# Kernel tuning notes

Measured on AMD Instinct MI355X. Metric: run time of the kernel, lower is better.

## Reference

```python
import jax, jax.numpy as jnp
import numpy as np

B, NS, D, H = 1024, 32, 1024, 4096
LN_EPS = 1e-5


def _layer_norm(x, g, b):
    mu = jnp.mean(x, axis=-1, keepdims=True)
    var = jnp.mean(jnp.square(x - mu), axis=-1, keepdims=True)
    return (x - mu) * jax.lax.rsqrt(var + LN_EPS) * g + b


def setup_inputs() -> dict:
    key = jax.random.key(0)
    ks = jax.random.split(key, 12)
    sc = 0.02
    inp = {
        "x": jax.random.normal(ks[0], (B, D), jnp.float32),
        "S": jax.random.normal(ks[1], (B, NS, D), jnp.float32),
        # route_mlp: Linear(2D, D) -> GELU -> Linear(D, NS)
        "w_r1": jax.random.normal(ks[2], (2 * D, D), jnp.float32) * sc,
        "b_r1": jnp.zeros((D,), jnp.float32),
        "w_r2": jax.random.normal(ks[3], (D, NS), jnp.float32) * sc,
        "b_r2": jnp.zeros((NS,), jnp.float32),
        # GRUCell(D, D): gates ordered [r, z, n] as in torch
        "w_ih": jax.random.normal(ks[4], (D, 3 * D), jnp.float32) * sc,
        "w_hh": jax.random.normal(ks[5], (D, 3 * D), jnp.float32) * sc,
        "b_ih": jnp.zeros((3 * D,), jnp.float32),
        "b_hh": jnp.zeros((3 * D,), jnp.float32),
        # slot_proj: Linear(D, D)
        "w_proj": jax.random.normal(ks[6], (D, D), jnp.float32) * sc,
        "b_proj": jnp.zeros((D,), jnp.float32),
        # ln1 / ffn / ln2
        "ln1_g": jnp.ones((D,), jnp.float32),
        "ln1_b": jnp.zeros((D,), jnp.float32),
        "w_f1": jax.random.normal(ks[7], (D, H), jnp.float32) * sc,
        "b_f1": jnp.zeros((H,), jnp.float32),
        "w_f2": jax.random.normal(ks[8], (H, D), jnp.float32) * sc,
        "b_f2": jnp.zeros((D,), jnp.float32),
        "ln2_g": jnp.ones((D,), jnp.float32),
        "ln2_b": jnp.zeros((D,), jnp.float32),
    }
    return inp


def reference(x, S, w_r1, b_r1, w_r2, b_r2, w_ih, w_hh, b_ih, b_hh,
              w_proj, b_proj, ln1_g, ln1_b, w_f1, b_f1, w_f2, b_f2,
              ln2_g, ln2_b):
    tau = 1.0
    # --- context-aware routing ---
    slot_mean = jnp.mean(S, axis=1)                     # [B, D]
    ctx = jnp.concatenate([x, slot_mean], axis=-1)      # [B, 2D]
    h_r = jax.nn.gelu(ctx @ w_r1 + b_r1, approximate=False)
    r_logits = h_r @ w_r2 + b_r2                        # [B, NS]
    alpha = jax.nn.softmax(r_logits / tau, axis=-1)     # [B, NS]

    # --- GRU slot update: input U = alpha * x broadcast over slots ---
    U = alpha[:, :, None] * x[:, None, :]               # [B, NS, D]
    gi = U @ w_ih + b_ih                                # [B, NS, 3D]
    gh = S @ w_hh + b_hh                                # [B, NS, 3D]
    gi_r, gi_z, gi_n = jnp.split(gi, 3, axis=-1)
    gh_r, gh_z, gh_n = jnp.split(gh, 3, axis=-1)
    r = jax.nn.sigmoid(gi_r + gh_r)
    z = jax.nn.sigmoid(gi_z + gh_z)
    n = jnp.tanh(gi_n + r * gh_n)
    S_new = (1.0 - z) * n + z * S                       # [B, NS, D]

    # --- weighted readout (slot_dropout = 0.0) ---
    slot_context = jnp.sum(alpha[:, :, None] * S_new, axis=1)  # [B, D]
    slot_update = slot_context @ w_proj + b_proj
    x_mid = x + slot_update

    # --- FFN + residual + LayerNorms ---
    h = _layer_norm(x_mid, ln1_g, ln1_b)
    ff = jax.nn.gelu(h @ w_f1 + b_f1, approximate=False) @ w_f2 + b_f2
    x_out = _layer_norm(x_mid + ff, ln2_g, ln2_b)
    return (x_out, S_new, alpha)
```

## Files before the change

kernel.cpp:

```cpp
#include <hip/hip_runtime.h>
#include <hip/hip_bf16.h>

#define BB 1024
#define NSLOT 32
#define DD 1024
#define HH 4096

typedef __bf16 bfx8 __attribute__((ext_vector_type(8)));
typedef float f32x4 __attribute__((ext_vector_type(4)));

__device__ __forceinline__ unsigned short f2bfu(float f) {
  union { float f; unsigned u; } v; v.f = f;
  unsigned r = v.u + 0x7fffu + ((v.u >> 16) & 1u);
  return (unsigned short)(r >> 16);
}
__device__ __forceinline__ float bfu2f(unsigned short u) {
  union { unsigned u; float f; } v; v.u = ((unsigned)u) << 16; return v.f;
}
__device__ __forceinline__ float gelu_f(float x) {
  return 0.5f * x * (1.0f + erff(x * 0.70710678118654752f));
}
__device__ __forceinline__ float sigm(float x) { return 1.0f / (1.0f + expf(-x)); }

__device__ __forceinline__ void async16(const unsigned short* g, unsigned short* l) {
  __builtin_amdgcn_global_load_lds(
      (const __attribute__((address_space(1))) unsigned int*)g,
      (__attribute__((address_space(3))) unsigned int*)l, 16, 0, 0);
}


__global__ __launch_bounds__(256) void cvt_x_ctx(const float* __restrict__ x,
                                                 unsigned short* __restrict__ ctx) {
  int i = blockIdx.x * 256 + threadIdx.x;
  int b = i >> 8;
  int c4 = (i & 255) * 4;
  float4 v = ((const float4*)(x + (size_t)b * DD))[i & 255];
  ushort4 o; o.x = f2bfu(v.x); o.y = f2bfu(v.y); o.z = f2bfu(v.z); o.w = f2bfu(v.w);
  *(ushort4*)&ctx[(size_t)b * (2 * DD) + c4] = o;
}

__global__ __launch_bounds__(256) void cvt4(const float* __restrict__ in,
                                            unsigned short* __restrict__ out, int n4) {
  int i = blockIdx.x * 256 + threadIdx.x;
  if (i >= n4) return;
  float4 v = ((const float4*)in)[i];
  ushort4 o; o.x = f2bfu(v.x); o.y = f2bfu(v.y); o.z = f2bfu(v.z); o.w = f2bfu(v.w);
  ((ushort4*)out)[i] = o;
}

__global__ __launch_bounds__(256) void slot_mean_k(const unsigned short* __restrict__ Sb,
                                                   unsigned short* __restrict__ ctx) {
  int i = blockIdx.x * 256 + threadIdx.x;
  int b = i >> 10, d = i & 1023;
  const unsigned short* p = Sb + (size_t)b * NSLOT * DD + d;
  float s = 0.f;
  #pragma unroll
  for (int sl = 0; sl < NSLOT; sl++) s += bfu2f(p[sl * DD]);
  ctx[(size_t)b * (2 * DD) + DD + d] = f2bfu(s * (1.0f / NSLOT));
}

__global__ __launch_bounds__(256) void transp(const float* __restrict__ in,
                                              unsigned short* __restrict__ out,
                                              int R, int C) {
  __shared__ float t[32][33];
  int tx = threadIdx.x & 31, ty = threadIdx.x >> 5;
  int c0 = blockIdx.x * 32, r0 = blockIdx.y * 32;
  #pragma unroll
  for (int i = 0; i < 4; i++) {
    int r = r0 + ty * 4 + i;
    t[ty * 4 + i][tx] = in[(size_t)r * C + c0 + tx];
  }
  __syncthreads();
  #pragma unroll
  for (int i = 0; i < 4; i++) {
    int c = c0 + ty * 4 + i;
    out[(size_t)c * R + r0 + tx] = f2bfu(t[tx][ty * 4 + i]);
  }
}

template <int EPI>
__global__ __launch_bounds__(256) void gemm_nt(
    const unsigned short* __restrict__ A, int lda,
    const unsigned short* __restrict__ Bt, int ldb, int K,
    const float* __restrict__ bias,
    const float* __restrict__ add, int ldadd,
    float* __restrict__ outF, unsigned short* __restrict__ outB, int ldout) {
  __shared__ __align__(16) unsigned short lA[128 * 40];
  __shared__ __align__(16) unsigned short lB[64 * 40];
  const int tid = threadIdx.x;
  const int wave = tid >> 6, lane = tid & 63;
  const int q = lane >> 4, l15 = lane & 15;
  const int row0 = blockIdx.y * 128;
  const int col0 = blockIdx.x * 64;
  const int ar = tid >> 2;
  const int ac = (tid & 3) * 8;

  f32x4 acc[2][4];
  #pragma unroll
  for (int m = 0; m < 2; m++)
    #pragma unroll
    for (int n = 0; n < 4; n++) acc[m][n] = (f32x4){0.f, 0.f, 0.f, 0.f};

  for (int k0 = 0; k0 < K; k0 += 32) {
    *(uint4*)&lA[ar * 40 + ac] = *(const uint4*)&A[(size_t)(row0 + ar) * lda + k0 + ac];
    *(uint4*)&lA[(ar + 64) * 40 + ac] = *(const uint4*)&A[(size_t)(row0 + ar + 64) * lda + k0 + ac];
    *(uint4*)&lB[ar * 40 + ac] = *(const uint4*)&Bt[(size_t)(col0 + ar) * ldb + k0 + ac];
    __syncthreads();
    bfx8 af[2], bf[4];
    #pragma unroll
    for (int m = 0; m < 2; m++)
      af[m] = *(const bfx8*)&lA[(wave * 32 + m * 16 + l15) * 40 + q * 8];
    #pragma unroll
    for (int n = 0; n < 4; n++)
      bf[n] = *(const bfx8*)&lB[(n * 16 + l15) * 40 + q * 8];
    #pragma unroll
    for (int m = 0; m < 2; m++)
      #pragma unroll
      for (int n = 0; n < 4; n++)
        acc[m][n] = __builtin_amdgcn_mfma_f32_16x16x32_bf16(af[m], bf[n], acc[m][n], 0, 0, 0);
    __syncthreads();
  }

  #pragma unroll
  for (int m = 0; m < 2; m++) {
    #pragma unroll
    for (int n = 0; n < 4; n++) {
      int gr0 = row0 + wave * 32 + m * 16 + q * 4;
      int gc = col0 + n * 16 + l15;
      #pragma unroll
      for (int i = 0; i < 4; i++) {
        int gr = gr0 + i;
        float v = acc[m][n][i];
        if (EPI == 0) {
          outF[(size_t)gr * ldout + gc] = v;
        } else if (EPI == 1) {
          float t = gelu_f(v + bias[gc]);
          outB[(size_t)gr * ldout + gc] = f2bfu(t);
        } else {
          outF[(size_t)gr * ldout + gc] = v + bias[gc] + add[(size_t)gr * ldadd + gc];
        }
      }
    }
  }
}

__global__ __launch_bounds__(256) void gru_gemm(
    const unsigned short* __restrict__ Sb, const unsigned short* __restrict__ Whht,
    const float* __restrict__ alpha, const float* __restrict__ xw,
    const float* __restrict__ b_ih, const float* __restrict__ b_hh,
    const float* __restrict__ Sf, float* __restrict__ Snew,
    unsigned short* __restrict__ sc_b) {
  __shared__ __align__(16) unsigned short lA[2][128 * 32];
  __shared__ __align__(16) unsigned short lB[2][192 * 32];
  const int tid = threadIdx.x;
  const int wave = tid >> 6, lane = tid & 63;
  const int wr = wave >> 1, wc = wave & 1;
  const int q = lane >> 4, l15 = lane & 15;
  const int row0 = blockIdx.y * 128;
  const int col0 = blockIdx.x * 64;
  const int halfA = 128 * 32, halfB = 192 * 32;

  const int lr = lane >> 2, scn = lane & 3;
  const unsigned short* aSrc[2];
  unsigned short* aDst[2];
  #pragma unroll
  for (int j = 0; j < 2; j++) {
    int R0 = (2 * wave + j) * 16;
    int r = R0 + lr;
    int c = scn ^ ((r >> 1) & 3);
    aSrc[j] = Sb + (size_t)(row0 + r) * DD + c * 8;
    aDst[j] = &lA[0][R0 * 32];
  }
  const unsigned short* bSrc[3];
  unsigned short* bDst[3];
  #pragma unroll
  for (int j = 0; j < 3; j++) {
    int R0 = (3 * wave + j) * 16;
    int r = R0 + lr;
    int g = r >> 6, cr = r & 63;
    int c = scn ^ ((r >> 1) & 3);
    bSrc[j] = Whht + ((size_t)g * DD + col0 + cr) * DD + c * 8;
    bDst[j] = &lB[0][R0 * 32];
  }

  int offA[4];
  #pragma unroll
  for (int m = 0; m < 4; m++) {
    int r = wr * 64 + m * 16 + l15;
    offA[m] = r * 32 + (q ^ ((r >> 1) & 3)) * 8;
  }
  int offB[3][2];
  #pragma unroll
  for (int g = 0; g < 3; g++)
    #pragma unroll
    for (int n = 0; n < 2; n++) {
      int r = g * 64 + wc * 32 + n * 16 + l15;
      offB[g][n] = r * 32 + (q ^ ((r >> 1) & 3)) * 8;
    }

  f32x4 acc[3][4][2];
  #pragma unroll
  for (int g = 0; g < 3; g++)
    #pragma unroll
    for (int m = 0; m < 4; m++)
      #pragma unroll
      for (int n = 0; n < 2; n++) acc[g][m][n] = (f32x4){0.f, 0.f, 0.f, 0.f};

  for (int it = 0; it < 16; it++) {
    #pragma unroll
    for (int j = 0; j < 2; j++) {
      async16(aSrc[j], aDst[j]);
      async16(aSrc[j] + 32, aDst[j] + halfA);
      aSrc[j] += 64;
    }
    #pragma unroll
    for (int j = 0; j < 3; j++) {
      async16(bSrc[j], bDst[j]);
      async16(bSrc[j] + 32, bDst[j] + halfB);
      bSrc[j] += 64;
    }
    __syncthreads();
    #pragma unroll
    for (int h = 0; h < 2; h++) {
      bfx8 af[4];
      #pragma unroll
      for (int m = 0; m < 4; m++) af[m] = *(const bfx8*)&lA[h][offA[m]];
      #pragma unroll
      for (int g = 0; g < 3; g++) {
        bfx8 bf0 = *(const bfx8*)&lB[h][offB[g][0]];
        bfx8 bf1 = *(const bfx8*)&lB[h][offB[g][1]];
        #pragma unroll
        for (int m = 0; m < 4; m++) {
          acc[g][m][0] = __builtin_amdgcn_mfma_f32_16x16x32_bf16(af[m], bf0, acc[g][m][0], 0, 0, 0);
          acc[g][m][1] = __builtin_amdgcn_mfma_f32_16x16x32_bf16(af[m], bf1, acc[g][m][1], 0, 0, 0);
        }
      }
    }
    __syncthreads();
  }

  float scp[2][2] = {{0.f, 0.f}, {0.f, 0.f}};
  #pragma unroll
  for (int m = 0; m < 4; m++) {
    #pragma unroll
    for (int i = 0; i < 4; i++) {
      int gr = row0 + wr * 64 + m * 16 + q * 4 + i;
      float a = alpha[gr];
      const float* xwr = xw + (size_t)(gr >> 5) * (3 * DD);
      const float* sfr = Sf + (size_t)gr * DD;
      float* orow = Snew + (size_t)gr * DD;
      #pragma unroll
      for (int n = 0; n < 2; n++) {
        int gc = col0 + wc * 32 + n * 16 + l15;
        float ghr = acc[0][m][n][i] + b_hh[gc];
        float ghz = acc[1][m][n][i] + b_hh[gc + DD];
        float ghn = acc[2][m][n][i] + b_hh[gc + 2 * DD];
        float r = sigm(a * xwr[gc] + b_ih[gc] + ghr);
        float z = sigm(a * xwr[gc + DD] + b_ih[gc + DD] + ghz);
        float nn = tanhf(a * xwr[gc + 2 * DD] + b_ih[gc + 2 * DD] + r * ghn);
        float sv = (1.0f - z) * nn + z * sfr[gc];
        orow[gc] = sv;
        scp[m >> 1][n] += a * sv;
      }
    }
  }
  #pragma unroll
  for (int bh = 0; bh < 2; bh++)
    #pragma unroll
    for (int n = 0; n < 2; n++) {
      float v = scp[bh][n];
      v += __shfl_xor(v, 16);
      v += __shfl_xor(v, 32);
      if (q == 0) {
        int batch = (row0 >> 5) + wr * 2 + bh;
        int gc = col0 + wc * 32 + n * 16 + l15;
        sc_b[(size_t)batch * DD + gc] = f2bfu(v);
      }
    }
}

__global__ __launch_bounds__(256) void route_softmax(
    const unsigned short* __restrict__ h_r, const float* __restrict__ w_r2,
    const float* __restrict__ b_r2, float* __restrict__ alpha_out) {
  int b = blockIdx.x;
  int n = threadIdx.x & 31, c = threadIdx.x >> 5;
  __shared__ float part[8][32];
  __shared__ float logits[32];
  const unsigned short* hr = h_r + (size_t)b * DD;
  float s = 0.f;
  for (int i = 0; i < 128; i++) {
    int k = c * 128 + i;
    s += bfu2f(hr[k]) * w_r2[k * NSLOT + n];
  }
  part[c][n] = s;
  __syncthreads();
  if (threadIdx.x < 32) {
    float t = b_r2[n];
    #pragma unroll
    for (int cc = 0; cc < 8; cc++) t += part[cc][n];
    logits[n] = t;
  }
  __syncthreads();
  if (threadIdx.x < 32) {
    float mx = -1e30f;
    #pragma unroll
    for (int j = 0; j < 32; j++) mx = fmaxf(mx, logits[j]);
    float den = 0.f;
    #pragma unroll
    for (int j = 0; j < 32; j++) den += expf(logits[j] - mx);
    alpha_out[(size_t)b * NSLOT + n] = expf(logits[n] - mx) / den;
  }
}

template <int OUT_BF>
__global__ __launch_bounds__(256) void ln_k(const float* __restrict__ in,
                                            const float* __restrict__ gw,
                                            const float* __restrict__ bw,
                                            float* __restrict__ outF,
                                            unsigned short* __restrict__ outB) {
  int b = blockIdx.x;
  int tid = threadIdx.x;
  float4 v = ((const float4*)(in + (size_t)b * DD))[tid];
  float s = v.x + v.y + v.z + v.w;
  float s2 = v.x * v.x + v.y * v.y + v.z * v.z + v.w * v.w;
  #pragma unroll
  for (int o = 32; o > 0; o >>= 1) { s += __shfl_down(s, o); s2 += __shfl_down(s2, o); }
  __shared__ float as1[4], as2[4];
  int wave = tid >> 6, lane = tid & 63;
  if (lane == 0) { as1[wave] = s; as2[wave] = s2; }
  __syncthreads();
  float t1 = as1[0] + as1[1] + as1[2] + as1[3];
  float t2 = as2[0] + as2[1] + as2[2] + as2[3];
  float mu = t1 * (1.0f / DD);
  float var = t2 * (1.0f / DD) - mu * mu;
  float rstd = rsqrtf(var + 1e-5f);
  int d = tid * 4;
  float o0 = (v.x - mu) * rstd * gw[d] + bw[d];
  float o1 = (v.y - mu) * rstd * gw[d + 1] + bw[d + 1];
  float o2 = (v.z - mu) * rstd * gw[d + 2] + bw[d + 2];
  float o3 = (v.w - mu) * rstd * gw[d + 3] + bw[d + 3];
  if (OUT_BF) {
    ushort4 o; o.x = f2bfu(o0); o.y = f2bfu(o1); o.z = f2bfu(o2); o.w = f2bfu(o3);
    *(ushort4*)&outB[(size_t)b * DD + d] = o;
  } else {
    float4 o; o.x = o0; o.y = o1; o.z = o2; o.w = o3;
    *(float4*)&outF[(size_t)b * DD + d] = o;
  }
}

extern "C" void kernel_launch(void* const* d_in, const int* in_sizes, int n_in,
                              void* d_out, int out_size, void* d_ws, size_t ws_size,
                              hipStream_t stream) {
  const float* x      = (const float*)d_in[0];
  const float* S      = (const float*)d_in[1];
  const float* w_r1   = (const float*)d_in[2];
  const float* b_r1   = (const float*)d_in[3];
  const float* w_r2   = (const float*)d_in[4];
  const float* b_r2   = (const float*)d_in[5];
  const float* w_ih   = (const float*)d_in[6];
  const float* w_hh   = (const float*)d_in[7];
  const float* b_ih   = (const float*)d_in[8];
  const float* b_hh   = (const float*)d_in[9];
  const float* w_proj = (const float*)d_in[10];
  const float* b_proj = (const float*)d_in[11];
  const float* ln1_g  = (const float*)d_in[12];
  const float* ln1_b  = (const float*)d_in[13];
  const float* w_f1   = (const float*)d_in[14];
  const float* b_f1   = (const float*)d_in[15];
  const float* w_f2   = (const float*)d_in[16];
  const float* b_f2   = (const float*)d_in[17];
  const float* ln2_g  = (const float*)d_in[18];
  const float* ln2_b  = (const float*)d_in[19];

  float* out_x = (float*)d_out;
  float* out_S = out_x + (size_t)BB * DD;
  float* out_a = out_S + (size_t)BB * NSLOT * DD;

  char* ws = (char*)d_ws;
  unsigned short* ctx    = (unsigned short*)(ws + 0);
  unsigned short* w_r1t  = (unsigned short*)(ws + 4194304);
  unsigned short* w_iht  = (unsigned short*)(ws + 8388608);
  unsigned short* w_hht  = (unsigned short*)(ws + 14680064);
  unsigned short* w_projt= (unsigned short*)(ws + 20971520);
  unsigned short* w_f1t  = (unsigned short*)(ws + 23068672);
  unsigned short* w_f2t  = (unsigned short*)(ws + 31457280);
  unsigned short* h_r    = (unsigned short*)(ws + 39845888);
  float*          xw     = (float*)(ws + 41943040);
  unsigned short* Sb     = (unsigned short*)(ws + 54525952);
  unsigned short* sc_b   = (unsigned short*)(ws + 0);
  float*          x_mid  = (float*)(ws + 41943040);
  unsigned short* h_ln   = (unsigned short*)(ws + 46137344);
  float*          pre2   = (float*)(ws + 48234496);
  unsigned short* ff1    = (unsigned short*)(ws + 54525952);

  dim3 blk(256);
  cvt_x_ctx<<<1024, blk, 0, stream>>>(x, ctx);
  cvt4<<<32768, blk, 0, stream>>>(S, Sb, (BB * NSLOT * DD) / 4);
  slot_mean_k<<<4096, blk, 0, stream>>>(Sb, ctx);
  transp<<<dim3(32, 64), blk, 0, stream>>>(w_r1, w_r1t, 2 * DD, DD);
  transp<<<dim3(96, 32), blk, 0, stream>>>(w_ih, w_iht, DD, 3 * DD);
  transp<<<dim3(96, 32), blk, 0, stream>>>(w_hh, w_hht, DD, 3 * DD);
  transp<<<dim3(32, 32), blk, 0, stream>>>(w_proj, w_projt, DD, DD);
  transp<<<dim3(128, 32), blk, 0, stream>>>(w_f1, w_f1t, DD, HH);
  transp<<<dim3(32, 128), blk, 0, stream>>>(w_f2, w_f2t, HH, DD);

  gemm_nt<1><<<dim3(16, 8), blk, 0, stream>>>(ctx, 2 * DD, w_r1t, 2 * DD, 2 * DD,
                                              b_r1, nullptr, 0, nullptr, h_r, DD);
  route_softmax<<<1024, blk, 0, stream>>>(h_r, w_r2, b_r2, out_a);

  gemm_nt<0><<<dim3(48, 8), blk, 0, stream>>>(ctx, 2 * DD, w_iht, DD, DD,
                                              nullptr, nullptr, 0, xw, nullptr, 3 * DD);

  gru_gemm<<<dim3(16, 256), blk, 0, stream>>>(Sb, w_hht, out_a, xw, b_ih, b_hh, S,
                                              out_S, sc_b);

  gemm_nt<2><<<dim3(16, 8), blk, 0, stream>>>(sc_b, DD, w_projt, DD, DD,
                                              b_proj, x, DD, x_mid, nullptr, DD);

  ln_k<1><<<1024, blk, 0, stream>>>(x_mid, ln1_g, ln1_b, nullptr, h_ln);
  gemm_nt<1><<<dim3(64, 8), blk, 0, stream>>>(h_ln, DD, w_f1t, DD, DD,
                                              b_f1, nullptr, 0, nullptr, ff1, HH);
  gemm_nt<2><<<dim3(16, 8), blk, 0, stream>>>(ff1, HH, w_f2t, HH, HH,
                                              b_f2, x_mid, DD, pre2, nullptr, DD);
  ln_k<0><<<1024, blk, 0, stream>>>(pre2, ln2_g, ln2_b, out_x, nullptr);
}
```

Before: 906.3 us.

## Double-buffer GRU GEMM LDS tiles and use fast sigmoid/tanh intrinsics

The GRU recurrent GEMM now keeps two LDS stage buffers. It issues the async global-to-LDS loads for the next K tile while MFMAs run on the current one, so memory latency is no longer exposed every iteration. The gate epilogue swaps expf/tanhf for hardware exp2 and rcp approximations to shorten the transcendental path. The LDS footprint doubles (to about 80KB), which can lower occupancy. The fast intrinsics also lose a little accuracy. Only one __syncthreads remains per iteration after compute, and the prefetch issued before it targets the other buffer, which relies on the barrier ordering being correct.

```diff
diff --git a/kernel.cpp b/kernel.cpp
--- a/kernel.cpp
+++ b/kernel.cpp
@@ -21,6 +21,14 @@
   return 0.5f * x * (1.0f + erff(x * 0.70710678118654752f));
 }
 __device__ __forceinline__ float sigm(float x) { return 1.0f / (1.0f + expf(-x)); }
+
+__device__ __forceinline__ float sigm_fast(float x) {
+  return __builtin_amdgcn_rcpf(1.0f + __builtin_amdgcn_exp2f(-1.4426950408889634f * x));
+}
+__device__ __forceinline__ float tanh_fast(float x) {
+  float t = __builtin_amdgcn_exp2f(2.8853900817779268f * x);
+  return 1.0f - 2.0f * __builtin_amdgcn_rcpf(1.0f + t);
+}
 
 __device__ __forceinline__ void async16(const unsigned short* g, unsigned short* l) {
   __builtin_amdgcn_global_load_lds(
@@ -150,29 +158,28 @@
     const float* __restrict__ b_ih, const float* __restrict__ b_hh,
     const float* __restrict__ Sf, float* __restrict__ Snew,
     unsigned short* __restrict__ sc_b) {
-  __shared__ __align__(16) unsigned short lA[2][128 * 32];
-  __shared__ __align__(16) unsigned short lB[2][192 * 32];
+  __shared__ __align__(16) unsigned short lA[2][2][128 * 32];
+  __shared__ __align__(16) unsigned short lB[2][2][192 * 32];
   const int tid = threadIdx.x;
   const int wave = tid >> 6, lane = tid & 63;
   const int wr = wave >> 1, wc = wave & 1;
   const int q = lane >> 4, l15 = lane & 15;
   const int row0 = blockIdx.y * 128;
   const int col0 = blockIdx.x * 64;
-  const int halfA = 128 * 32, halfB = 192 * 32;
 
   const int lr = lane >> 2, scn = lane & 3;
   const unsigned short* aSrc[2];
-  unsigned short* aDst[2];
+  int aOff[2];
   #pragma unroll
   for (int j = 0; j < 2; j++) {
     int R0 = (2 * wave + j) * 16;
     int r = R0 + lr;
     int c = scn ^ ((r >> 1) & 3);
     aSrc[j] = Sb + (size_t)(row0 + r) * DD + c * 8;
-    aDst[j] = &lA[0][R0 * 32];
+    aOff[j] = R0 * 32;
   }
   const unsigned short* bSrc[3];
-  unsigned short* bDst[3];
+  int bOff[3];
   #pragma unroll
   for (int j = 0; j < 3; j++) {
     int R0 = (3 * wave + j) * 16;
@@ -180,7 +187,7 @@
     int g = r >> 6, cr = r & 63;
     int c = scn ^ ((r >> 1) & 3);
     bSrc[j] = Whht + ((size_t)g * DD + col0 + cr) * DD + c * 8;
-    bDst[j] = &lB[0][R0 * 32];
+    bOff[j] = R0 * 32;
   }
 
   int offA[4];
@@ -206,29 +213,46 @@
       #pragma unroll
       for (int n = 0; n < 2; n++) acc[g][m][n] = (f32x4){0.f, 0.f, 0.f, 0.f};
 
+  #pragma unroll
+  for (int j = 0; j < 2; j++) {
+    async16(aSrc[j], &lA[0][0][aOff[j]]);
+    async16(aSrc[j] + 32, &lA[0][1][aOff[j]]);
+    aSrc[j] += 64;
+  }
+  #pragma unroll
+  for (int j = 0; j < 3; j++) {
+    async16(bSrc[j], &lB[0][0][bOff[j]]);
+    async16(bSrc[j] + 32, &lB[0][1][bOff[j]]);
+    bSrc[j] += 64;
+  }
+  __syncthreads();
+
   for (int it = 0; it < 16; it++) {
-    #pragma unroll
-    for (int j = 0; j < 2; j++) {
-      async16(aSrc[j], aDst[j]);
-      async16(aSrc[j] + 32, aDst[j] + halfA);
-      aSrc[j] += 64;
-    }
-    #pragma unroll
-    for (int j = 0; j < 3; j++) {
-      async16(bSrc[j], bDst[j]);
-      async16(bSrc[j] + 32, bDst[j] + halfB);
-      bSrc[j] += 64;
-    }
-    __syncthreads();
+    const int buf = it & 1;
+    if (it < 15) {
+      const int nb = buf ^ 1;
+      #pragma unroll
+      for (int j = 0; j < 2; j++) {
+        async16(aSrc[j], &lA[nb][0][aOff[j]]);
+        async16(aSrc[j] + 32, &lA[nb][1][aOff[j]]);
+        aSrc[j] += 64;
+      }
+      #pragma unroll
+      for (int j = 0; j < 3; j++) {
+        async16(bSrc[j], &lB[nb][0][bOff[j]]);
+        async16(bSrc[j] + 32, &lB[nb][1][bOff[j]]);
+        bSrc[j] += 64;
+      }
+    }
     #pragma unroll
     for (int h = 0; h < 2; h++) {
       bfx8 af[4];
       #pragma unroll
-      for (int m = 0; m < 4; m++) af[m] = *(const bfx8*)&lA[h][offA[m]];
+      for (int m = 0; m < 4; m++) af[m] = *(const bfx8*)&lA[buf][h][offA[m]];
       #pragma unroll
       for (int g = 0; g < 3; g++) {
-        bfx8 bf0 = *(const bfx8*)&lB[h][offB[g][0]];
-        bfx8 bf1 = *(const bfx8*)&lB[h][offB[g][1]];
+        bfx8 bf0 = *(const bfx8*)&lB[buf][h][offB[g][0]];
+        bfx8 bf1 = *(const bfx8*)&lB[buf][h][offB[g][1]];
         #pragma unroll
         for (int m = 0; m < 4; m++) {
           acc[g][m][0] = __builtin_amdgcn_mfma_f32_16x16x32_bf16(af[m], bf0, acc[g][m][0], 0, 0, 0);
@@ -255,9 +279,9 @@
         float ghr = acc[0][m][n][i] + b_hh[gc];
         float ghz = acc[1][m][n][i] + b_hh[gc + DD];
         float ghn = acc[2][m][n][i] + b_hh[gc + 2 * DD];
-        float r = sigm(a * xwr[gc] + b_ih[gc] + ghr);
-        float z = sigm(a * xwr[gc + DD] + b_ih[gc + DD] + ghz);
-        float nn = tanhf(a * xwr[gc + 2 * DD] + b_ih[gc + 2 * DD] + r * ghn);
+        float r = sigm_fast(a * xwr[gc] + b_ih[gc] + ghr);
+        float z = sigm_fast(a * xwr[gc + DD] + b_ih[gc + DD] + ghz);
+        float nn = tanh_fast(a * xwr[gc + 2 * DD] + b_ih[gc + 2 * DD] + r * ghn);
         float sv = (1.0f - z) * nn + z * sfr[gc];
         orow[gc] = sv;
         scp[m >> 1][n] += a * sv;
```

After: 1.009 ms. 1.11x slower.
